# Kernel optimization log

Measured on AMD Instinct MI355X. Metric: run time of the kernel, lower is better.

Reference implementation:

```python
import jax, jax.numpy as jnp
import numpy as np

E, K, N, T, TOPK, GROUP_SIZE = 8, 2048, 2048, 1024, 2, 128


def setup_inputs() -> dict:
    key = jax.random.key(0)
    ks = jax.random.split(key, 6)
    x = jax.random.normal(ks[0], (T, K), dtype=jnp.float32)
    # uint8-quantized weights stored as int32 (values 0..255)
    w_q = jax.random.randint(ks[1], (E, K, N), 0, 256, dtype=jnp.int32)
    scales = jax.random.uniform(ks[2], (E, K, K // GROUP_SIZE), dtype=jnp.float32) * 0.02
    zeros = jax.random.normal(ks[3], (E, K, K // GROUP_SIZE), dtype=jnp.float32) * 0.1
    topk_weights = jax.random.uniform(ks[4], (T, TOPK), dtype=jnp.float32)
    topk_ids = jax.random.randint(ks[5], (T, TOPK), 0, E, dtype=jnp.int32)
    return {"x": x, "w_q": w_q, "scales": scales, "zeros": zeros,
            "topk_weights": topk_weights, "topk_ids": topk_ids}


def reference(x, w_q, scales, zeros, topk_weights, topk_ids):
    # Faithful to _moe_kernel_w8a16: for each (token, expert-slot) pair,
    #   out[t, n] += topk_weight * sum_k x[t, k] * (w_q[e, k, n] * scales[e, k, k//gs] + zeros[e, k, k//gs])
    # Note the kernel broadcasts scale/zero over n (offs_n * 0) with group index k // group_size.
    k_idx = jnp.arange(K)
    g_idx = k_idx // GROUP_SIZE                      # (K,)
    s = scales[:, k_idx, g_idx]                       # (E, K) scale per (e, k)
    z = zeros[:, k_idx, g_idx]                        # (E, K)
    w_deq = w_q.astype(jnp.float32) * s[:, :, None] + z[:, :, None]  # (E, K, N)
    # dense per-expert GEMM, then gather the top_k experts per token
    all_out = jnp.einsum('tk,ekn->ten', x, w_deq)     # (T, E, N)
    sel = jnp.take_along_axis(all_out, topk_ids[:, :, None].astype(jnp.int32), axis=1)  # (T, TOPK, N)
    out = jnp.sum(sel * topk_weights[:, :, None], axis=1)  # (T, N)
    return out
```

## Files before the change

kernel.cpp:

```cpp
#include <hip/hip_runtime.h>
#include <hip/hip_bf16.h>
#include <stdint.h>

#define E_    8
#define K_    2048
#define N_    2048
#define T_    1024
#define TOPK_ 2
#define NG_   16
#define MAXM  512

#define BM 128
#define BN 64
#define BK 64
#define KSPLIT 2
#define KCHUNK (K_ / KSPLIT)
#define NST (KCHUNK / BK)
#define MTILES 3

typedef __attribute__((ext_vector_type(8))) short bf16x8;
typedef __attribute__((ext_vector_type(4))) float f32x4;
typedef __attribute__((ext_vector_type(4))) unsigned int u32x4;
typedef __attribute__((ext_vector_type(8))) unsigned short u16x8;

__device__ __forceinline__ unsigned short f2bf_rne(float f) {
    unsigned u = __float_as_uint(f);
    u += 0x7fffu + ((u >> 16) & 1u);
    return (unsigned short)(u >> 16);
}
__device__ __forceinline__ unsigned short f2bf_trunc(float f) {
    return (unsigned short)(__float_as_uint(f) >> 16);
}

__device__ __forceinline__ void gload_lds16(const void* g, void* l) {
    __builtin_amdgcn_global_load_lds(
        (__attribute__((address_space(1))) unsigned int*)g,
        (__attribute__((address_space(3))) unsigned int*)l,
        16, 0, 0);
}

__global__ void prep_sz(const float* __restrict__ scales, const float* __restrict__ zeros,
                        float* __restrict__ sd, float* __restrict__ zd, int* __restrict__ cnt)
{
    int i = blockIdx.x * 256 + threadIdx.x;
    int e = i >> 11;
    int k = i & (K_ - 1);
    int g = k >> 7;
    size_t src = ((size_t)e * K_ + k) * NG_ + g;
    sd[i] = scales[src];
    zd[i] = zeros[src];
    if (i < E_) cnt[i] = 0;
}

__global__ void route_k(const int* __restrict__ topk_ids, int* __restrict__ cnt,
                        int* __restrict__ ptj)
{
    int idx = blockIdx.x * 256 + threadIdx.x;
    if (idx < T_ * TOPK_) {
        int e = topk_ids[idx];
        int slot = atomicAdd(&cnt[e], 1);
        if (slot < T_ * TOPK_) ptj[e * (T_ * TOPK_) + slot] = idx;
    }
}

__global__ void zdot_k(const float* __restrict__ x, const float* __restrict__ zdiag,
                       const int* __restrict__ topk_ids, float* __restrict__ zdot)
{
    int w = (int)((blockIdx.x * blockDim.x + threadIdx.x) >> 6);
    int lane = threadIdx.x & 63;
    int t = w >> 1;
    int e = topk_ids[w];
    const f32x4* xp = (const f32x4*)(x + (size_t)t * K_);
    const f32x4* zp = (const f32x4*)(zdiag + (size_t)e * K_);
    float acc = 0.f;
#pragma unroll
    for (int it = 0; it < K_ / 256; ++it) {
        f32x4 a = xp[it * 64 + lane];
        f32x4 b = zp[it * 64 + lane];
        acc += a.x * b.x + a.y * b.y + a.z * b.z + a.w * b.w;
    }
#pragma unroll
    for (int off = 32; off > 0; off >>= 1) acc += __shfl_xor(acc, off);
    if (lane == 0) zdot[w] = acc;
}

__global__ void aprep_k(const float* __restrict__ x, const float* __restrict__ sdiag,
                        const int* __restrict__ cnt, const int* __restrict__ ptj,
                        unsigned short* __restrict__ apack)
{
    int e = blockIdx.y;
    int slot = blockIdx.x;
    if (slot >= min(cnt[e], MAXM)) return;
    int tj = ptj[e * (T_ * TOPK_) + slot];
    int t = tj >> 1;
    const float* xr = x + (size_t)t * K_;
    const float* sr = sdiag + (size_t)e * K_;
    int k = threadIdx.x * 8;
    f32x4 a0 = *(const f32x4*)(xr + k);
    f32x4 s0 = *(const f32x4*)(sr + k);
    f32x4 a1 = *(const f32x4*)(xr + k + 4);
    f32x4 s1 = *(const f32x4*)(sr + k + 4);
    u16x8 h;
    h[0] = f2bf_rne(a0.x * s0.x);
    h[1] = f2bf_rne(a0.y * s0.y);
    h[2] = f2bf_rne(a0.z * s0.z);
    h[3] = f2bf_rne(a0.w * s0.w);
    h[4] = f2bf_rne(a1.x * s1.x);
    h[5] = f2bf_rne(a1.y * s1.y);
    h[6] = f2bf_rne(a1.z * s1.z);
    h[7] = f2bf_rne(a1.w * s1.w);
    *(u16x8*)(apack + ((size_t)e * MAXM + slot) * K_ + k) = h;
}

__global__ __launch_bounds__(256, 3)
void moe_gemm(const int* __restrict__ wq, const unsigned short* __restrict__ apack,
              const float* __restrict__ topk_w, const int* __restrict__ cnt,
              const int* __restrict__ ptj, const float* __restrict__ zdot,
              float* __restrict__ out)
{
    int bz = blockIdx.z;
    int e = bz >> 1;
    int ks = bz & 1;
    int k0 = ks * KCHUNK;
    int count = min(cnt[e], MAXM);
    int m0 = blockIdx.y * BM;
    if (m0 >= count) return;
    int n0 = blockIdx.x * BN;

    __shared__ alignas(16) unsigned short As[2][BM * BK];
    __shared__ alignas(16) unsigned short Bs[2][BN * BK];

    int tid = threadIdx.x;
    int lane = tid & 63;
    int wid = tid >> 6;
    int wm = (wid >> 1) * 64;
    int wn = (wid & 1) * 32;

    int lrow = lane >> 3;
    int lcol = lane & 7;
    int aswz = (lcol ^ lrow) << 4;
    const char* abase = (const char*)(apack + (size_t)e * MAXM * K_);

    int b_n = tid & 63;
    int b_set = tid >> 6;
    const int* wcol = wq + (size_t)e * K_ * N_ + n0 + b_n;
    int bswz = (b_n & 7) << 4;

    f32x4 acc[4][2] = {};
    int ba[16], bb[16];

    auto stageA = [&](int buf, int kt) {
        int kk = k0 + kt * BK;
#pragma unroll
        for (int ci = 0; ci < 4; ++ci) {
            int c = wid * 4 + ci;
            int p = m0 + c * 8 + lrow;
            const char* g = abase + ((size_t)p * K_ + kk) * 2 + aswz;
            gload_lds16(g, (char*)As[buf] + c * 1024);
        }
    };
    auto loadB = [&](int* br, int kt) {
        int kb = k0 + kt * BK + b_set * 16;
#pragma unroll
        for (int i = 0; i < 16; ++i)
            br[i] = wcol[(kb + i) * N_];
    };
    auto packB = [&](const int* br, int buf) {
        unsigned pk[8];
#pragma unroll
        for (int i = 0; i < 8; ++i) {
            unsigned lo = f2bf_trunc((float)br[2 * i]);
            unsigned hi = f2bf_trunc((float)br[2 * i + 1]);
            pk[i] = lo | (hi << 16);
        }
        char* bsrow = (char*)Bs[buf] + b_n * (BK * 2);
#pragma unroll
        for (int seg = 0; seg < 2; ++seg) {
            int kbyte = b_set * 32 + seg * 16;
            u32x4 v = { pk[seg * 4], pk[seg * 4 + 1], pk[seg * 4 + 2], pk[seg * 4 + 3] };
            *(u32x4*)(bsrow + (kbyte ^ bswz)) = v;
        }
    };
    auto comp = [&](int buf) {
#pragma unroll
        for (int kk2 = 0; kk2 < 2; ++kk2) {
            int kb = kk2 * 64 + ((lane >> 4) << 4);
            bf16x8 af[4], bfr[2];
#pragma unroll
            for (int mi = 0; mi < 4; ++mi) {
                int row = wm + mi * 16 + (lane & 15);
                af[mi] = *(const bf16x8*)((const char*)As[buf] + row * 128 + (kb ^ ((row & 7) << 4)));
            }
#pragma unroll
            for (int ni = 0; ni < 2; ++ni) {
                int row = wn + ni * 16 + (lane & 15);
                bfr[ni] = *(const bf16x8*)((const char*)Bs[buf] + row * 128 + (kb ^ ((row & 7) << 4)));
            }
#pragma unroll
            for (int mi = 0; mi < 4; ++mi)
#pragma unroll
                for (int ni = 0; ni < 2; ++ni)
                    acc[mi][ni] = __builtin_amdgcn_mfma_f32_16x16x32_bf16(
                        af[mi], bfr[ni], acc[mi][ni], 0, 0, 0);
        }
    };

    stageA(0, 0);
    __builtin_amdgcn_sched_barrier(0);
    loadB(ba, 0);
    loadB(bb, 1);
    packB(ba, 0);
    asm volatile("s_waitcnt vmcnt(16) lgkmcnt(0)" ::: "memory");
    __builtin_amdgcn_s_barrier();
    __builtin_amdgcn_sched_barrier(0);

#pragma unroll 1
    for (int it = 0; it < 7; ++it) {
        int u = 2 * it;
        stageA(1, u + 1);
        __builtin_amdgcn_sched_barrier(0);
        loadB(ba, u + 2);
        comp(0);
        packB(bb, 1);
        asm volatile("s_waitcnt vmcnt(16) lgkmcnt(0)" ::: "memory");
        __builtin_amdgcn_s_barrier();
        __builtin_amdgcn_sched_barrier(0);
        stageA(0, u + 2);
        __builtin_amdgcn_sched_barrier(0);
        loadB(bb, u + 3);
        comp(1);
        packB(ba, 0);
        asm volatile("s_waitcnt vmcnt(16) lgkmcnt(0)" ::: "memory");
        __builtin_amdgcn_s_barrier();
        __builtin_amdgcn_sched_barrier(0);
    }
    stageA(1, 15);
    comp(0);
    packB(bb, 1);
    asm volatile("s_waitcnt vmcnt(0) lgkmcnt(0)" ::: "memory");
    __builtin_amdgcn_s_barrier();
    __builtin_amdgcn_sched_barrier(0);
    comp(1);

#pragma unroll
    for (int mi = 0; mi < 4; ++mi) {
        int prow = m0 + wm + mi * 16 + ((lane >> 4) << 2);
#pragma unroll
        for (int r = 0; r < 4; ++r) {
            int p = prow + r;
            if (p < count) {
                int tj = ptj[e * (T_ * TOPK_) + p];
                int tok = tj >> 1;
                float w = topk_w[tj];
                float zdv = ks ? 0.f : zdot[tj];
                float* orow = out + (size_t)tok * N_ + n0 + wn + (lane & 15);
#pragma unroll
                for (int ni = 0; ni < 2; ++ni)
                    atomicAdd(orow + ni * 16, w * (acc[mi][ni][r] + zdv));
            }
        }
    }
}

extern "C" void kernel_launch(void* const* d_in, const int* in_sizes, int n_in,
                              void* d_out, int out_size, void* d_ws, size_t ws_size,
                              hipStream_t stream)
{
    const float* x       = (const float*)d_in[0];
    const int*   wq      = (const int*)d_in[1];
    const float* scales  = (const float*)d_in[2];
    const float* zeros   = (const float*)d_in[3];
    const float* topk_w  = (const float*)d_in[4];
    const int*   topk_id = (const int*)d_in[5];
    float* out = (float*)d_out;

    char* ws = (char*)d_ws;
    float* sdiag = (float*)(ws + 0);
    float* zdiag = (float*)(ws + 65536);
    int*   cnt   = (int*)(ws + 131072);
    int*   ptj   = (int*)(ws + 135168);
    float* zdot  = (float*)(ws + 200704);
    unsigned short* apack = (unsigned short*)(ws + (1 << 20));

    hipMemsetAsync(d_out, 0, (size_t)T_ * N_ * sizeof(float), stream);
    prep_sz<<<E_ * K_ / 256, 256, 0, stream>>>(scales, zeros, sdiag, zdiag, cnt);
    route_k<<<T_ * TOPK_ / 256, 256, 0, stream>>>(topk_id, cnt, ptj);
    zdot_k<<<T_ * TOPK_ / 4, 256, 0, stream>>>(x, zdiag, topk_id, zdot);
    aprep_k<<<dim3(MAXM, E_), 256, 0, stream>>>(x, sdiag, cnt, ptj, apack);
    moe_gemm<<<dim3(N_ / BN, MTILES, E_ * KSPLIT), 256, 0, stream>>>(
        wq, apack, topk_w, cnt, ptj, zdot, out);
}
```

Baseline: 97.88 us.

## Drop K-split, deepen B register prefetch, replace output atomics with partial-sum reduce

The GEMM no longer splits K across two blocks. Each block now runs the full K loop, using three rotating register buffers for the uint8 weight loads so B is fetched two steps ahead. When the workspace is large enough, each (token, slot) row is written to a partial buffer without atomics, and a separate reduce kernel sums the two slots per token. That path also removes the output memset. The trade-off is half as many blocks along K, which means less parallelism and longer blocks, plus an extra kernel launch and extra partial-buffer traffic.

New measurement: 83.41 us. -14.8%, faster.

```diff
diff --git a/kernel.cpp b/kernel.cpp
--- a/kernel.cpp
+++ b/kernel.cpp
@@ -13,10 +13,8 @@
 #define BM 128
 #define BN 64
 #define BK 64
-#define KSPLIT 2
-#define KCHUNK (K_ / KSPLIT)
-#define NST (KCHUNK / BK)
-#define MTILES 3
+#define NST (K_ / BK)
+#define MTILES (MAXM / BM)
 
 typedef __attribute__((ext_vector_type(8))) short bf16x8;
 typedef __attribute__((ext_vector_type(4))) float f32x4;
@@ -116,12 +114,9 @@
 void moe_gemm(const int* __restrict__ wq, const unsigned short* __restrict__ apack,
               const float* __restrict__ topk_w, const int* __restrict__ cnt,
               const int* __restrict__ ptj, const float* __restrict__ zdot,
-              float* __restrict__ out)
-{
-    int bz = blockIdx.z;
-    int e = bz >> 1;
-    int ks = bz & 1;
-    int k0 = ks * KCHUNK;
+              float* __restrict__ part, float* __restrict__ out, int use_part)
+{
+    int e = blockIdx.z;
     int count = min(cnt[e], MAXM);
     int m0 = blockIdx.y * BM;
     if (m0 >= count) return;
@@ -147,10 +142,10 @@
     int bswz = (b_n & 7) << 4;
 
     f32x4 acc[4][2] = {};
-    int ba[16], bb[16];
+    int b0[16], b1[16], b2[16];
 
     auto stageA = [&](int buf, int kt) {
-        int kk = k0 + kt * BK;
+        int kk = kt * BK;
 #pragma unroll
         for (int ci = 0; ci < 4; ++ci) {
             int c = wid * 4 + ci;
@@ -160,7 +155,7 @@
         }
     };
     auto loadB = [&](int* br, int kt) {
-        int kb = k0 + kt * BK + b_set * 16;
+        int kb = kt * BK + b_set * 16;
 #pragma unroll
         for (int i = 0; i < 16; ++i)
             br[i] = wcol[(kb + i) * N_];
@@ -207,36 +202,53 @@
 
     stageA(0, 0);
     __builtin_amdgcn_sched_barrier(0);
-    loadB(ba, 0);
-    loadB(bb, 1);
-    packB(ba, 0);
-    asm volatile("s_waitcnt vmcnt(16) lgkmcnt(0)" ::: "memory");
+    loadB(b0, 0);
+    loadB(b1, 1);
+    loadB(b2, 2);
+    packB(b0, 0);
+    asm volatile("s_waitcnt vmcnt(32) lgkmcnt(0)" ::: "memory");
     __builtin_amdgcn_s_barrier();
     __builtin_amdgcn_sched_barrier(0);
 
+    int kt = 0;
+#define STEP(C, BL, BP) do {                                                  \
+        stageA(C ^ 1, kt + 1);                                                \
+        __builtin_amdgcn_sched_barrier(0);                                    \
+        loadB(BL, kt + 3);                                                    \
+        comp(C);                                                              \
+        packB(BP, C ^ 1);                                                     \
+        asm volatile("s_waitcnt vmcnt(16) lgkmcnt(0)" ::: "memory");          \
+        __builtin_amdgcn_s_barrier();                                         \
+        __builtin_amdgcn_sched_barrier(0);                                    \
+        ++kt;                                                                 \
+    } while (0)
+
 #pragma unroll 1
-    for (int it = 0; it < 7; ++it) {
-        int u = 2 * it;
-        stageA(1, u + 1);
-        __builtin_amdgcn_sched_barrier(0);
-        loadB(ba, u + 2);
-        comp(0);
-        packB(bb, 1);
-        asm volatile("s_waitcnt vmcnt(16) lgkmcnt(0)" ::: "memory");
-        __builtin_amdgcn_s_barrier();
-        __builtin_amdgcn_sched_barrier(0);
-        stageA(0, u + 2);
-        __builtin_amdgcn_sched_barrier(0);
-        loadB(bb, u + 3);
-        comp(1);
-        packB(ba, 0);
-        asm volatile("s_waitcnt vmcnt(16) lgkmcnt(0)" ::: "memory");
-        __builtin_amdgcn_s_barrier();
-        __builtin_amdgcn_sched_barrier(0);
+    for (int it = 0; it < 4; ++it) {
+        STEP(0, b0, b1);
+        STEP(1, b1, b2);
+        STEP(0, b2, b0);
+        STEP(1, b0, b1);
+        STEP(0, b1, b2);
+        STEP(1, b2, b0);
     }
-    stageA(1, 15);
+    STEP(0, b0, b1);
+    STEP(1, b1, b2);
+    STEP(0, b2, b0);
+    STEP(1, b0, b1);
+    STEP(0, b1, b2);
+#undef STEP
+    stageA(0, 30);
+    __builtin_amdgcn_sched_barrier(0);
+    comp(1);
+    packB(b0, 0);
+    asm volatile("s_waitcnt vmcnt(0) lgkmcnt(0)" ::: "memory");
+    __builtin_amdgcn_s_barrier();
+    __builtin_amdgcn_sched_barrier(0);
+    stageA(1, 31);
+    __builtin_amdgcn_sched_barrier(0);
     comp(0);
-    packB(bb, 1);
+    packB(b1, 1);
     asm volatile("s_waitcnt vmcnt(0) lgkmcnt(0)" ::: "memory");
     __builtin_amdgcn_s_barrier();
     __builtin_amdgcn_sched_barrier(0);
@@ -250,16 +262,32 @@
             int p = prow + r;
             if (p < count) {
                 int tj = ptj[e * (T_ * TOPK_) + p];
-                int tok = tj >> 1;
                 float w = topk_w[tj];
-                float zdv = ks ? 0.f : zdot[tj];
-                float* orow = out + (size_t)tok * N_ + n0 + wn + (lane & 15);
-#pragma unroll
-                for (int ni = 0; ni < 2; ++ni)
-                    atomicAdd(orow + ni * 16, w * (acc[mi][ni][r] + zdv));
+                float zdv = zdot[tj];
+                float v0 = w * (acc[mi][0][r] + zdv);
+                float v1 = w * (acc[mi][1][r] + zdv);
+                if (use_part) {
+                    float* pr = part + (size_t)tj * N_ + n0 + wn + (lane & 15);
+                    pr[0]  = v0;
+                    pr[16] = v1;
+                } else {
+                    float* orow = out + (size_t)(tj >> 1) * N_ + n0 + wn + (lane & 15);
+                    atomicAdd(orow + 0,  v0);
+                    atomicAdd(orow + 16, v1);
+                }
             }
         }
     }
+}
+
+__global__ void reduce_k(const float* __restrict__ part, float* __restrict__ out)
+{
+    int g = blockIdx.x * 256 + threadIdx.x;
+    int t = g >> 9;
+    int nc = g & 511;
+    f32x4 a = ((const f32x4*)part)[((size_t)(t * 2) << 9) + nc];
+    f32x4 b = ((const f32x4*)part)[((size_t)(t * 2 + 1) << 9) + nc];
+    ((f32x4*)out)[g] = a + b;
 }
 
 extern "C" void kernel_launch(void* const* d_in, const int* in_sizes, int n_in,
@@ -281,12 +309,18 @@
     int*   ptj   = (int*)(ws + 135168);
     float* zdot  = (float*)(ws + 200704);
     unsigned short* apack = (unsigned short*)(ws + (1 << 20));
-
-    hipMemsetAsync(d_out, 0, (size_t)T_ * N_ * sizeof(float), stream);
+    float* part  = (float*)(ws + ((size_t)17 << 20));
+    size_t need = ((size_t)17 << 20) + (size_t)T_ * TOPK_ * N_ * sizeof(float);
+    int use_part = (ws_size >= need) ? 1 : 0;
+
     prep_sz<<<E_ * K_ / 256, 256, 0, stream>>>(scales, zeros, sdiag, zdiag, cnt);
     route_k<<<T_ * TOPK_ / 256, 256, 0, stream>>>(topk_id, cnt, ptj);
     zdot_k<<<T_ * TOPK_ / 4, 256, 0, stream>>>(x, zdiag, topk_id, zdot);
     aprep_k<<<dim3(MAXM, E_), 256, 0, stream>>>(x, sdiag, cnt, ptj, apack);
-    moe_gemm<<<dim3(N_ / BN, MTILES, E_ * KSPLIT), 256, 0, stream>>>(
-        wq, apack, topk_w, cnt, ptj, zdot, out);
-}
+    if (!use_part)
+        hipMemsetAsync(d_out, 0, (size_t)T_ * N_ * sizeof(float), stream);
+    moe_gemm<<<dim3(N_ / BN, MTILES, E_), 256, 0, stream>>>(
+        wq, apack, topk_w, cnt, ptj, zdot, part, out, use_part);
+    if (use_part)
+        reduce_k<<<T_ * N_ / 4 / 256, 256, 0, stream>>>(part, out);
+}
```
